# Kernel tuning notes

Hardware: AMD Instinct MI355X
Metric: run time of the kernel (lower is better)

Reference implementation:

```python
import jax, jax.numpy as jnp
import numpy as np

V, D, H, DH, DI, L = 10000, 512, 8, 64, 2048, 12
B, S = 4, 1024
MAX_KLEN = 1024 + 0 + 512  # tgt_len + ext_len + mem_len
EPS = 1e-5
STD = 0.02


def setup_inputs() -> dict:
    key = jax.random.key(0)
    ks = jax.random.split(key, 10)
    data = jax.random.randint(ks[0], (B, S), 0, V)
    word_emb = jax.random.normal(ks[1], (V, D), jnp.float32) * STD
    pos_emb = jax.random.normal(ks[2], (MAX_KLEN, D), jnp.float32) * STD
    Wq = jax.random.normal(ks[3], (L, H * DH, D), jnp.float32) * STD
    Wkv = jax.random.normal(ks[4], (L, 2 * H * DH, D), jnp.float32) * STD
    Wo = jax.random.normal(ks[5], (L, D, H * DH), jnp.float32) * STD
    ln1_g = jnp.ones((L, D), jnp.float32)
    ln1_b = jnp.zeros((L, D), jnp.float32)
    W1 = jax.random.normal(ks[6], (L, DI, D), jnp.float32) * STD
    b1 = jnp.zeros((L, DI), jnp.float32)
    W2 = jax.random.normal(ks[7], (L, D, DI), jnp.float32) * STD
    b2 = jnp.zeros((L, D), jnp.float32)
    ln2_g = jnp.ones((L, D), jnp.float32)
    ln2_b = jnp.zeros((L, D), jnp.float32)
    out_b = jnp.zeros((V,), jnp.float32)  # out_layer weight is tied to word_emb
    return dict(data=data, word_emb=word_emb, pos_emb=pos_emb, Wq=Wq, Wkv=Wkv,
                Wo=Wo, ln1_g=ln1_g, ln1_b=ln1_b, W1=W1, b1=b1, W2=W2, b2=b2,
                ln2_g=ln2_g, ln2_b=ln2_b, out_b=out_b)


def _layernorm(x, g, b):
    m = jnp.mean(x, axis=-1, keepdims=True)
    v = jnp.mean((x - m) ** 2, axis=-1, keepdims=True)
    return (x - m) * jax.lax.rsqrt(v + EPS) * g + b


def reference(data, word_emb, pos_emb, Wq, Wkv, Wo, ln1_g, ln1_b,
              W1, b1, W2, b2, ln2_g, ln2_b, out_b):
    # mems start empty -> mlen = 0, klen = qlen, standard causal mask.
    h = word_emb[data] + pos_emb[:S][None, :, :]      # [B, S, D]
    mask = jnp.triu(jnp.ones((S, S), bool), 1)        # True above diagonal
    scale = 1.0 / np.sqrt(DH)

    def layer(h, p):
        wq, wkv, wo, g1, bl1, w1, bf1, w2, bf2, g2, bl2 = p
        q = (h @ wq.T).reshape(B, S, H, DH)
        k, v = jnp.split(h @ wkv.T, 2, axis=-1)
        k = k.reshape(B, S, H, DH)
        v = v.reshape(B, S, H, DH)
        sc = jnp.einsum('bqhd,bkhd->bhqk', q, k) * scale
        sc = jnp.where(mask[None, None], -jnp.inf, sc)
        p_attn = jax.nn.softmax(sc, axis=-1)           # [B, H, S, S] materialized
        av = jnp.einsum('bhqk,bkhd->bqhd', p_attn, v).reshape(B, S, H * DH)
        h = _layernorm(h + av @ wo.T, g1, bl1)         # post-LN (pre_lnorm=False)
        ff = jax.nn.relu(h @ w1.T + bf1) @ w2.T + bf2
        h = _layernorm(h + ff, g2, bl2)
        return h, None

    h, _ = jax.lax.scan(layer, h,
                        (Wq, Wkv, Wo, ln1_g, ln1_b, W1, b1, W2, b2, ln2_g, ln2_b))
    logits = h @ word_emb.T + out_b                    # tied output projection
    return logits                                      # [B, S, V]
```

## Files before the change

kernel.cpp:

```cpp
#include <hip/hip_runtime.h>

#define VV 10000
#define DD 512
#define HH 8
#define DH 64
#define DI 2048
#define LL 12
#define BB 4
#define SS 1024
#define TT (BB * SS)


typedef __attribute__((ext_vector_type(8))) short bhalf8;
typedef __attribute__((ext_vector_type(16))) float f32x16;

__device__ __forceinline__ void split_bf16(float x, unsigned short& h, unsigned short& l)
{
    unsigned int u = __float_as_uint(x);
    unsigned int r = (u + 0x7FFFu + ((u >> 16) & 1u)) & 0xFFFF0000u;
    h = (unsigned short)(r >> 16);
    float lf = x - __uint_as_float(r);
    unsigned int ul = __float_as_uint(lf);
    l = (unsigned short)((ul + 0x7FFFu + ((ul >> 16) & 1u)) >> 16);
}

__global__ __launch_bounds__(256) void convsplit(
    const float* __restrict__ src, unsigned short* __restrict__ hi,
    unsigned short* __restrict__ lo, int n4)
{
    int stride = gridDim.x * 256;
    for (int i = blockIdx.x * 256 + threadIdx.x; i < n4; i += stride) {
        float4 v = ((const float4*)src)[i];
        ushort4 h, l;
        split_bf16(v.x, h.x, l.x);
        split_bf16(v.y, h.y, l.y);
        split_bf16(v.z, h.z, l.z);
        split_bf16(v.w, h.w, l.w);
        ((ushort4*)hi)[i] = h;
        ((ushort4*)lo)[i] = l;
    }
}

__global__ __launch_bounds__(256) void embed_kernel(
    const int* __restrict__ data, const float* __restrict__ we,
    const float* __restrict__ pe, float* __restrict__ h,
    unsigned short* __restrict__ hhi, unsigned short* __restrict__ hlo)
{
    int tok = blockIdx.x;
    int tid = threadIdx.x;
    int idx = data[tok];
    int s = tok & (SS - 1);
    size_t base = (size_t)tok * DD;
    size_t wb = (size_t)idx * DD;
    size_t pb = (size_t)s * DD;
    float a = we[wb + tid] + pe[pb + tid];
    float b = we[wb + 256 + tid] + pe[pb + 256 + tid];
    h[base + tid] = a;
    h[base + 256 + tid] = b;
    unsigned short hx, lx;
    split_bf16(a, hx, lx); hhi[base + tid] = hx;       hlo[base + tid] = lx;
    split_bf16(b, hx, lx); hhi[base + 256 + tid] = hx; hlo[base + 256 + tid] = lx;
}

template<int BN, int EPI, bool SWZ>
__global__ __launch_bounds__(256) void gemm_mfma(
    const unsigned short* __restrict__ Ahp, const unsigned short* __restrict__ Alp,
    const unsigned short* __restrict__ Whp, const unsigned short* __restrict__ Wlp,
    const float* __restrict__ bias, float* __restrict__ C,
    unsigned short* __restrict__ Chp, unsigned short* __restrict__ Clp,
    unsigned short* __restrict__ Vhp, unsigned short* __restrict__ Vlp,
    int N, int K)
{
    constexpr int FN  = BN / 64;
    constexpr int BT  = BN * 128;
    constexpr int NBG = BN / 8;
    constexpr int NGRP = 32 + 2 * NBG;
    constexpr int PW  = NGRP / 4;
    __shared__ __align__(16) char smem[32768 + 2 * BT];

    int bx = blockIdx.x, by = blockIdx.y;
    if (SWZ) {
        int nwg = gridDim.x * gridDim.y;
        int id = by * gridDim.x + bx;
        int nq = nwg >> 3, rr = nwg & 7;
        int xcd = id & 7, j = id >> 3;
        int nid = (xcd < rr) ? (xcd * (nq + 1) + j)
                             : (rr * (nq + 1) + (xcd - rr) * nq + j);
        bx = nid % gridDim.x;
        by = nid / gridDim.x;
    }

    const int tid   = threadIdx.x;
    const int lane  = tid & 63;
    const int wid   = tid >> 6;
    const int wm    = wid >> 1;
    const int wn    = wid & 1;
    const int laneM = lane & 31;
    const int laneK = lane >> 5;
    const int m0    = by * 128;
    const int n0    = bx * BN;
    const int srow8 = lane >> 3;
    const int sslot = lane & 7;

    f32x16 acc[2][FN];
    #pragma unroll
    for (int i = 0; i < 2; ++i)
        #pragma unroll
        for (int j = 0; j < FN; ++j)
            #pragma unroll
            for (int r = 0; r < 16; ++r) acc[i][j][r] = 0.f;

    for (int k0 = 0; k0 < K; k0 += 64) {
        __syncthreads();
        bhalf8 rbuf[PW];
        #pragma unroll
        for (int t = 0; t < PW; ++t) {
            int g = wid * PW + t;
            const unsigned short* src;
            if (g < 32) {
                const unsigned short* bp = (g < 16) ? Ahp : Alp;
                int row = (g & 15) * 8 + srow8;
                src = bp + (size_t)(m0 + row) * K + (k0 + sslot * 8);
            } else {
                int d = g - 32;
                const unsigned short* bp = (d < NBG) ? Whp : Wlp;
                int row = (d & (NBG - 1)) * 8 + srow8;
                int n = n0 + row;
                n = (n < N) ? n : (N - 1);
                src = bp + (size_t)n * K + (k0 + sslot * 8);
            }
            rbuf[t] = *(const bhalf8*)src;
        }
        #pragma unroll
        for (int t = 0; t < PW; ++t) {
            int g = wid * PW + t;
            int off;
            if (g < 32) {
                int row = (g & 15) * 8 + srow8;
                off = ((g >> 4) << 14) + sslot * 2048 + ((row ^ sslot) << 4);
            } else {
                int d = g - 32;
                int row = (d & (NBG - 1)) * 8 + srow8;
                off = 32768 + ((d < NBG) ? 0 : BT)
                    + sslot * (BN * 16) + ((row ^ sslot) << 4);
            }
            *(bhalf8*)(smem + off) = rbuf[t];
        }
        __syncthreads();

        #pragma unroll
        for (int kb = 0; kb < 4; ++kb) {
            const int slot = kb * 2 + laneK;
            bhalf8 ah[2], al[2], bh[FN], bl[FN];
            #pragma unroll
            for (int i = 0; i < 2; ++i) {
                int row = wm * 64 + i * 32 + laneM;
                int off = slot * 2048 + ((row ^ slot) << 4);
                ah[i] = *(const bhalf8*)(smem + off);
                al[i] = *(const bhalf8*)(smem + 16384 + off);
            }
            #pragma unroll
            for (int j = 0; j < FN; ++j) {
                int row = wn * (BN / 2) + j * 32 + laneM;
                int off = 32768 + slot * (BN * 16) + ((row ^ slot) << 4);
                bh[j] = *(const bhalf8*)(smem + off);
                bl[j] = *(const bhalf8*)(smem + BT + off);
            }
            #pragma unroll
            for (int i = 0; i < 2; ++i)
                #pragma unroll
                for (int j = 0; j < FN; ++j) {
                    acc[i][j] = __builtin_amdgcn_mfma_f32_32x32x16_bf16(ah[i], bh[j], acc[i][j], 0, 0, 0);
                    acc[i][j] = __builtin_amdgcn_mfma_f32_32x32x16_bf16(ah[i], bl[j], acc[i][j], 0, 0, 0);
                    acc[i][j] = __builtin_amdgcn_mfma_f32_32x32x16_bf16(al[i], bh[j], acc[i][j], 0, 0, 0);
                }
        }
    }

    #pragma unroll
    for (int j = 0; j < FN; ++j) {
        int ncol = n0 + wn * (BN / 2) + j * 32 + laneM;
        bool nok = (ncol < N);
        float bv = 0.f;
        if (EPI == 1 || EPI == 2) { if (nok) bv = bias[ncol]; }
        #pragma unroll
        for (int i = 0; i < 2; ++i) {
            #pragma unroll
            for (int r = 0; r < 16; ++r) {
                int mrow = m0 + wm * 64 + i * 32 + (r & 3) + ((r >> 2) << 3) + laneK * 4;
                float v = acc[i][j][r] + bv;
                if (EPI == 2) v = fmaxf(v, 0.f);
                if (nok) {
                    if (EPI == 2 || EPI == 3) {
                        unsigned short hx, lx;
                        split_bf16(v, hx, lx);
                        Chp[(size_t)mrow * N + ncol] = hx;
                        Clp[(size_t)mrow * N + ncol] = lx;
                    } else if (EPI == 4) {
                        unsigned short hx, lx;
                        split_bf16(v, hx, lx);
                        if (ncol < 512) {
                            Chp[(size_t)mrow * 512 + ncol] = hx;
                            Clp[(size_t)mrow * 512 + ncol] = lx;
                        } else {
                            Vhp[(size_t)(ncol - 512) * TT + mrow] = hx;
                            Vlp[(size_t)(ncol - 512) * TT + mrow] = lx;
                        }
                    } else {
                        C[(size_t)mrow * N + ncol] = v;
                    }
                }
            }
        }
    }
}

__global__ __launch_bounds__(128) void flash_mfma(
    const unsigned short* __restrict__ qhp, const unsigned short* __restrict__ qlp,
    const unsigned short* __restrict__ khp, const unsigned short* __restrict__ klp,
    const unsigned short* __restrict__ vthp, const unsigned short* __restrict__ vtlp,
    unsigned short* __restrict__ avh, unsigned short* __restrict__ avl)
{
    __shared__ __align__(16) char lds[50176];

    const int qt  = 15 - (int)blockIdx.x;
    const int hh  = blockIdx.y;
    const int b   = blockIdx.z;
    const int tid = threadIdx.x;
    const int lane  = tid & 63;
    const int wq    = tid >> 6;
    const int laneM = lane & 31;
    const int laneK = lane >> 5;
    const int q0    = qt * 64;

    bhalf8 Qh[4], Ql[4];
    {
        size_t qoff = (size_t)(b * SS + q0 + 32 * wq + laneM) * 512 + hh * 64 + 8 * laneK;
        #pragma unroll
        for (int ks = 0; ks < 4; ++ks) {
            Qh[ks] = *(const bhalf8*)(qhp + qoff + 16 * ks);
            Ql[ks] = *(const bhalf8*)(qlp + qoff + 16 * ks);
        }
    }

    f32x16 O0, O1;
    #pragma unroll
    for (int r = 0; r < 16; ++r) { O0[r] = 0.f; O1[r] = 0.f; }
    float mrun = -1e30f, lrun = 0.f;

    const int srow  = tid >> 1;
    const int shalf = tid & 1;
    float* Pl = (float*)(lds + 32768 + wq * 8704);

    for (int kt = 0; kt <= qt; ++kt) {
        __syncthreads();
        {
            size_t kbase = (size_t)(b * SS + kt * 64 + srow) * 512 + hh * 64 + 32 * shalf;
            size_t vbase = (size_t)(hh * 64 + srow) * TT + b * SS + kt * 64 + 32 * shalf;
            bhalf8 k0[4], k1[4], v0[4], v1[4];
            #pragma unroll
            for (int j = 0; j < 4; ++j) {
                k0[j] = *(const bhalf8*)(khp  + kbase + 8 * j);
                k1[j] = *(const bhalf8*)(klp  + kbase + 8 * j);
                v0[j] = *(const bhalf8*)(vthp + vbase + 8 * j);
                v1[j] = *(const bhalf8*)(vtlp + vbase + 8 * j);
            }
            int ob = srow * 128 + 64 * shalf;
            int sw = (srow & 7) << 4;
            #pragma unroll
            for (int j = 0; j < 4; ++j) {
                int o = (ob + 16 * j) ^ sw;
                *(bhalf8*)(lds + o)         = k0[j];
                *(bhalf8*)(lds + 8192 + o)  = k1[j];
                *(bhalf8*)(lds + 16384 + o) = v0[j];
                *(bhalf8*)(lds + 24576 + o) = v1[j];
            }
        }
        __syncthreads();

        f32x16 s0, s1;
        #pragma unroll
        for (int r = 0; r < 16; ++r) { s0[r] = 0.f; s1[r] = 0.f; }
        #pragma unroll
        for (int ks = 0; ks < 4; ++ks) {
            int db = 32 * ks + 16 * laneK;
            int o0 = (laneM * 128 + db) ^ ((laneM & 7) << 4);
            int r1 = 32 + laneM;
            int o1 = (r1 * 128 + db) ^ ((r1 & 7) << 4);
            bhalf8 kh0 = *(const bhalf8*)(lds + o0);
            bhalf8 kl0 = *(const bhalf8*)(lds + 8192 + o0);
            bhalf8 kh1 = *(const bhalf8*)(lds + o1);
            bhalf8 kl1 = *(const bhalf8*)(lds + 8192 + o1);
            s0 = __builtin_amdgcn_mfma_f32_32x32x16_bf16(kh0, Qh[ks], s0, 0, 0, 0);
            s0 = __builtin_amdgcn_mfma_f32_32x32x16_bf16(kh0, Ql[ks], s0, 0, 0, 0);
            s0 = __builtin_amdgcn_mfma_f32_32x32x16_bf16(kl0, Qh[ks], s0, 0, 0, 0);
            s1 = __builtin_amdgcn_mfma_f32_32x32x16_bf16(kh1, Qh[ks], s1, 0, 0, 0);
            s1 = __builtin_amdgcn_mfma_f32_32x32x16_bf16(kh1, Ql[ks], s1, 0, 0, 0);
            s1 = __builtin_amdgcn_mfma_f32_32x32x16_bf16(kl1, Qh[ks], s1, 0, 0, 0);
        }

        #pragma unroll
        for (int r = 0; r < 16; ++r) { s0[r] *= 0.125f; s1[r] *= 0.125f; }

        if (kt == qt) {
            int qrel = 32 * wq + laneM;
            #pragma unroll
            for (int r = 0; r < 16; ++r) {
                int krel = (r & 3) + ((r >> 2) << 3) + 4 * laneK;
                if (krel > qrel)      s0[r] = -1e30f;
                if (krel + 32 > qrel) s1[r] = -1e30f;
            }
        }

        float mx = s0[0];
        #pragma unroll
        for (int r = 1; r < 16; ++r) mx = fmaxf(mx, s0[r]);
        #pragma unroll
        for (int r = 0; r < 16; ++r) mx = fmaxf(mx, s1[r]);
        mx = fmaxf(mx, __shfl_xor(mx, 32));
        float mn = fmaxf(mrun, mx);
        float alpha = __expf(mrun - mn);
        mrun = mn;
        float rs = 0.f;
        #pragma unroll
        for (int r = 0; r < 16; ++r) {
            float p0 = __expf(s0[r] - mn);
            float p1 = __expf(s1[r] - mn);
            s0[r] = p0; s1[r] = p1;
            rs += p0 + p1;
        }
        rs += __shfl_xor(rs, 32);
        lrun = lrun * alpha + rs;
        #pragma unroll
        for (int r = 0; r < 16; ++r) { O0[r] *= alpha; O1[r] *= alpha; }

        #pragma unroll
        for (int r = 0; r < 16; ++r) {
            int krel = (r & 3) + ((r >> 2) << 3) + 4 * laneK;
            Pl[laneM * 68 + krel]      = s0[r];
            Pl[laneM * 68 + 32 + krel] = s1[r];
        }
        __asm__ volatile("s_waitcnt lgkmcnt(0)" ::: "memory");
        __builtin_amdgcn_sched_barrier(0);

        #pragma unroll
        for (int ks = 0; ks < 4; ++ks) {
            const float* pr = &Pl[laneM * 68 + 16 * ks + 8 * laneK];
            float4 pa = *(const float4*)pr;
            float4 pb = *(const float4*)(pr + 4);
            float pv[8] = {pa.x, pa.y, pa.z, pa.w, pb.x, pb.y, pb.z, pb.w};
            bhalf8 ph, plo;
            #pragma unroll
            for (int i = 0; i < 8; ++i) {
                unsigned u = __float_as_uint(pv[i]);
                ph[i] = (short)(u >> 16);
                float lf = pv[i] - __uint_as_float(u & 0xFFFF0000u);
                plo[i] = (short)(__float_as_uint(lf) >> 16);
            }
            int db = 32 * ks + 16 * laneK;
            {
                int col = laneM;
                int o = (col * 128 + db) ^ ((col & 7) << 4);
                bhalf8 vh = *(const bhalf8*)(lds + 16384 + o);
                bhalf8 vl = *(const bhalf8*)(lds + 24576 + o);
                O0 = __builtin_amdgcn_mfma_f32_32x32x16_bf16(vh, ph,  O0, 0, 0, 0);
                O0 = __builtin_amdgcn_mfma_f32_32x32x16_bf16(vl, ph,  O0, 0, 0, 0);
                O0 = __builtin_amdgcn_mfma_f32_32x32x16_bf16(vh, plo, O0, 0, 0, 0);
            }
            {
                int col = 32 + laneM;
                int o = (col * 128 + db) ^ ((col & 7) << 4);
                bhalf8 vh = *(const bhalf8*)(lds + 16384 + o);
                bhalf8 vl = *(const bhalf8*)(lds + 24576 + o);
                O1 = __builtin_amdgcn_mfma_f32_32x32x16_bf16(vh, ph,  O1, 0, 0, 0);
                O1 = __builtin_amdgcn_mfma_f32_32x32x16_bf16(vl, ph,  O1, 0, 0, 0);
                O1 = __builtin_amdgcn_mfma_f32_32x32x16_bf16(vh, plo, O1, 0, 0, 0);
            }
        }
    }

    float inv = 1.0f / lrun;
    #pragma unroll
    for (int r = 0; r < 16; ++r) {
        int d = (r & 3) + ((r >> 2) << 3) + 4 * laneK;
        Pl[laneM * 68 + d]      = O0[r] * inv;
        Pl[laneM * 68 + 32 + d] = O1[r] * inv;
    }
    __asm__ volatile("s_waitcnt lgkmcnt(0)" ::: "memory");
    __builtin_amdgcn_sched_barrier(0);
    #pragma unroll
    for (int it = 0; it < 16; ++it) {
        int qr = it * 2 + (lane >> 5);
        int d  = (lane & 31) * 2;
        float2 v = *(const float2*)&Pl[qr * 68 + d];
        unsigned short h0, l0, h1, l1;
        split_bf16(v.x, h0, l0);
        split_bf16(v.y, h1, l1);
        size_t base = (size_t)(b * SS + q0 + 32 * wq + qr) * 512 + hh * 64 + d;
        ushort2 hv; hv.x = h0; hv.y = h1;
        ushort2 lv; lv.x = l0; lv.y = l1;
        *(ushort2*)(avh + base) = hv;
        *(ushort2*)(avl + base) = lv;
    }
}

__global__ __launch_bounds__(256) void add_ln_kernel(
    float* __restrict__ h, const float* __restrict__ x,
    const float* __restrict__ g, const float* __restrict__ bta,
    unsigned short* __restrict__ hhi, unsigned short* __restrict__ hlo)
{
    int tok = blockIdx.x, tid = threadIdx.x;
    size_t base = (size_t)tok * DD;
    float v0 = h[base + tid] + x[base + tid];
    float v1 = h[base + 256 + tid] + x[base + 256 + tid];

    __shared__ float rs[256], rq[256];
    rs[tid] = v0 + v1;
    rq[tid] = v0 * v0 + v1 * v1;
    __syncthreads();
    for (int off = 128; off > 0; off >>= 1) {
        if (tid < off) { rs[tid] += rs[tid + off]; rq[tid] += rq[tid + off]; }
        __syncthreads();
    }
    float mean = rs[0] * (1.f / 512.f);
    float var  = rq[0] * (1.f / 512.f) - mean * mean;
    float inv  = rsqrtf(var + 1e-5f);
    float o0 = (v0 - mean) * inv * g[tid]       + bta[tid];
    float o1 = (v1 - mean) * inv * g[256 + tid] + bta[256 + tid];
    h[base + tid]       = o0;
    h[base + 256 + tid] = o1;
    unsigned short a, b;
    split_bf16(o0, a, b); hhi[base + tid]       = a; hlo[base + tid]       = b;
    split_bf16(o1, a, b); hhi[base + 256 + tid] = a; hlo[base + 256 + tid] = b;
}

extern "C" void kernel_launch(void* const* d_in, const int* in_sizes, int n_in,
                              void* d_out, int out_size, void* d_ws, size_t ws_size,
                              hipStream_t stream)
{
    const int*   data = (const int*)d_in[0];
    const float* we   = (const float*)d_in[1];
    const float* pe   = (const float*)d_in[2];
    const float* Wq   = (const float*)d_in[3];
    const float* Wkv  = (const float*)d_in[4];
    const float* Wo   = (const float*)d_in[5];
    const float* g1   = (const float*)d_in[6];
    const float* bl1  = (const float*)d_in[7];
    const float* W1   = (const float*)d_in[8];
    const float* b1   = (const float*)d_in[9];
    const float* W2   = (const float*)d_in[10];
    const float* b2   = (const float*)d_in[11];
    const float* g2   = (const float*)d_in[12];
    const float* bl2  = (const float*)d_in[13];
    const float* outb = (const float*)d_in[14];
    float* out = (float*)d_out;

    typedef unsigned short us;
    float* h    = (float*)d_ws;
    us* qhp  = (us*)(h + (size_t)TT * 512);
    us* qlp  = qhp  + (size_t)TT * 512;
    us* khp  = qlp  + (size_t)TT * 512;
    us* klp  = khp  + (size_t)TT * 512;
    us* vthp = klp  + (size_t)TT * 512;
    us* vtlp = vthp + (size_t)TT * 512;
    us* avh  = vtlp + (size_t)TT * 512;
    us* avl  = avh  + (size_t)TT * 512;
    float* tmp = (float*)(avl + (size_t)TT * 512);
    us* hhi  = (us*)(tmp + (size_t)TT * 512);
    us* hlo  = hhi + (size_t)TT * 512;
    us* ffh = qhp;
    us* ffl = qhp + (size_t)TT * 2048;
    us* wqh  = hlo + (size_t)TT * 512;
    us* wql  = wqh  + (size_t)LL * 512 * 512;
    us* wkvh = wql  + (size_t)LL * 512 * 512;
    us* wkvl = wkvh + (size_t)LL * 1024 * 512;
    us* woh  = wkvl + (size_t)LL * 1024 * 512;
    us* wol  = woh  + (size_t)LL * 512 * 512;
    us* w1h  = wol  + (size_t)LL * 512 * 512;
    us* w1l  = w1h  + (size_t)LL * 2048 * 512;
    us* w2h  = w1l  + (size_t)LL * 2048 * 512;
    us* w2l  = w2h  + (size_t)LL * 512 * 2048;
    us* weh  = w2l  + (size_t)LL * 512 * 2048;
    us* wel  = weh  + (size_t)VV * 512;

    auto cv = [&](const float* s, us* hh, us* ll, size_t n) {
        int n4 = (int)(n >> 2);
        int blocks = (n4 + 255) / 256;
        if (blocks > 2048) blocks = 2048;
        convsplit<<<blocks, 256, 0, stream>>>(s, hh, ll, n4);
    };
    cv(Wq,  wqh,  wql,  (size_t)LL * 512 * 512);
    cv(Wkv, wkvh, wkvl, (size_t)LL * 1024 * 512);
    cv(Wo,  woh,  wol,  (size_t)LL * 512 * 512);
    cv(W1,  w1h,  w1l,  (size_t)LL * 2048 * 512);
    cv(W2,  w2h,  w2l,  (size_t)LL * 512 * 2048);
    cv(we,  weh,  wel,  (size_t)VV * 512);

    embed_kernel<<<TT, 256, 0, stream>>>(data, we, pe, h, hhi, hlo);

    for (int l = 0; l < LL; ++l) {
        const us* lwqh  = wqh  + (size_t)l * 512 * 512;
        const us* lwql  = wql  + (size_t)l * 512 * 512;
        const us* lwkvh = wkvh + (size_t)l * 1024 * 512;
        const us* lwkvl = wkvl + (size_t)l * 1024 * 512;
        const us* lwoh  = woh  + (size_t)l * 512 * 512;
        const us* lwol  = wol  + (size_t)l * 512 * 512;
        const us* lw1h  = w1h  + (size_t)l * 2048 * 512;
        const us* lw1l  = w1l  + (size_t)l * 2048 * 512;
        const us* lw2h  = w2h  + (size_t)l * 512 * 2048;
        const us* lw2l  = w2l  + (size_t)l * 512 * 2048;

        gemm_mfma<64, 3, false><<<dim3(8, 32), 256, 0, stream>>>(
            hhi, hlo, lwqh, lwql, nullptr, nullptr, qhp, qlp, nullptr, nullptr, 512, 512);
        gemm_mfma<128, 4, false><<<dim3(8, 32), 256, 0, stream>>>(
            hhi, hlo, lwkvh, lwkvl, nullptr, nullptr, khp, klp, vthp, vtlp, 1024, 512);
        flash_mfma<<<dim3(16, HH, BB), 128, 0, stream>>>(
            qhp, qlp, khp, klp, vthp, vtlp, avh, avl);
        gemm_mfma<64, 0, false><<<dim3(8, 32), 256, 0, stream>>>(
            avh, avl, lwoh, lwol, nullptr, tmp, nullptr, nullptr, nullptr, nullptr, 512, 512);
        add_ln_kernel<<<TT, 256, 0, stream>>>(h, tmp, g1 + l * 512, bl1 + l * 512, hhi, hlo);
        gemm_mfma<128, 2, false><<<dim3(16, 32), 256, 0, stream>>>(
            hhi, hlo, lw1h, lw1l, b1 + l * 2048, nullptr, ffh, ffl, nullptr, nullptr, 2048, 512);
        gemm_mfma<64, 1, false><<<dim3(8, 32), 256, 0, stream>>>(
            ffh, ffl, lw2h, lw2l, b2 + l * 512, tmp, nullptr, nullptr, nullptr, nullptr, 512, 2048);
        add_ln_kernel<<<TT, 256, 0, stream>>>(h, tmp, g2 + l * 512, bl2 + l * 512, hhi, hlo);
    }

    gemm_mfma<128, 1, true><<<dim3((VV + 127) / 128, 32), 256, 0, stream>>>(
        hhi, hlo, weh, wel, outb, out, nullptr, nullptr, nullptr, nullptr, VV, 512);
}
```

Baseline: 3.500 ms.

## Prefetch GEMM tiles into registers, hardcode XCD swizzle, raise MFMA priority

The GEMM main loop now issues next-iteration global loads into registers right after the LDS store, so they overlap with the MFMA compute. Load offsets and LDS addresses are precomputed once, using 32-bit offsets from the Ahp base. The XCD-aware block swizzle is replaced by a hardcoded mapping that assumes a 79-wide grid with 10-column groups. Attention MFMA sections are wrapped in s_setprio to favor matrix-issuing waves. The hardcoded swizzle only fits one grid shape and may mis-map blocks for any other SWZ launch, and the int offsets could overflow on large buffers.

```diff
diff --git a/kernel.cpp b/kernel.cpp
--- a/kernel.cpp
+++ b/kernel.cpp
@@ -80,14 +80,10 @@
 
     int bx = blockIdx.x, by = blockIdx.y;
     if (SWZ) {
-        int nwg = gridDim.x * gridDim.y;
-        int id = by * gridDim.x + bx;
-        int nq = nwg >> 3, rr = nwg & 7;
-        int xcd = id & 7, j = id >> 3;
-        int nid = (xcd < rr) ? (xcd * (nq + 1) + j)
-                             : (rr * (nq + 1) + (xcd - rr) * nq + j);
-        bx = nid % gridDim.x;
-        by = nid / gridDim.x;
+        int id = by * 79 + bx;
+        int t  = (id & 7) * 316 + (id >> 3);
+        if (t < 2240) { int c = t / 320, r = t - c * 320; by = r / 10; bx = c * 10 + r % 10; }
+        else          { int r = t - 2240;                 by = r / 9;  bx = 70 + r % 9; }
     }
 
     const int tid   = threadIdx.x;
@@ -102,6 +98,29 @@
     const int srow8 = lane >> 3;
     const int sslot = lane & 7;
 
+    const int dAl = (int)(Alp - Ahp);
+    const int dW  = (int)(Whp - Ahp);
+    const int dWl = (int)(Wlp - Ahp);
+    int offs[PW];
+    int ldso[PW];
+    #pragma unroll
+    for (int t = 0; t < PW; ++t) {
+        int g = wid * PW + t;
+        if (g < 32) {
+            int row = (g & 15) * 8 + srow8;
+            offs[t] = (g < 16 ? 0 : dAl) + (m0 + row) * K + sslot * 8;
+            ldso[t] = ((g >> 4) << 14) + sslot * 2048 + ((row ^ sslot) << 4);
+        } else {
+            int d = g - 32;
+            int row = (d & (NBG - 1)) * 8 + srow8;
+            int n = n0 + row;
+            n = (n < N) ? n : (N - 1);
+            offs[t] = (d < NBG ? dW : dWl) + n * K + sslot * 8;
+            ldso[t] = 32768 + ((d < NBG) ? 0 : BT)
+                    + sslot * (BN * 16) + ((row ^ sslot) << 4);
+        }
+    }
+
     f32x16 acc[2][FN];
     #pragma unroll
     for (int i = 0; i < 2; ++i)
@@ -109,44 +128,24 @@
         for (int j = 0; j < FN; ++j)
             #pragma unroll
             for (int r = 0; r < 16; ++r) acc[i][j][r] = 0.f;
+
+    bhalf8 rbuf[PW];
+    #pragma unroll
+    for (int t = 0; t < PW; ++t)
+        rbuf[t] = *(const bhalf8*)(Ahp + offs[t]);
 
     for (int k0 = 0; k0 < K; k0 += 64) {
         __syncthreads();
-        bhalf8 rbuf[PW];
-        #pragma unroll
-        for (int t = 0; t < PW; ++t) {
-            int g = wid * PW + t;
-            const unsigned short* src;
-            if (g < 32) {
-                const unsigned short* bp = (g < 16) ? Ahp : Alp;
-                int row = (g & 15) * 8 + srow8;
-                src = bp + (size_t)(m0 + row) * K + (k0 + sslot * 8);
-            } else {
-                int d = g - 32;
-                const unsigned short* bp = (d < NBG) ? Whp : Wlp;
-                int row = (d & (NBG - 1)) * 8 + srow8;
-                int n = n0 + row;
-                n = (n < N) ? n : (N - 1);
-                src = bp + (size_t)n * K + (k0 + sslot * 8);
-            }
-            rbuf[t] = *(const bhalf8*)src;
-        }
-        #pragma unroll
-        for (int t = 0; t < PW; ++t) {
-            int g = wid * PW + t;
-            int off;
-            if (g < 32) {
-                int row = (g & 15) * 8 + srow8;
-                off = ((g >> 4) << 14) + sslot * 2048 + ((row ^ sslot) << 4);
-            } else {
-                int d = g - 32;
-                int row = (d & (NBG - 1)) * 8 + srow8;
-                off = 32768 + ((d < NBG) ? 0 : BT)
-                    + sslot * (BN * 16) + ((row ^ sslot) << 4);
-            }
-            *(bhalf8*)(smem + off) = rbuf[t];
-        }
+        #pragma unroll
+        for (int t = 0; t < PW; ++t)
+            *(bhalf8*)(smem + ldso[t]) = rbuf[t];
         __syncthreads();
+
+        if (k0 + 64 < K) {
+            #pragma unroll
+            for (int t = 0; t < PW; ++t)
+                rbuf[t] = *(const bhalf8*)(Ahp + offs[t] + k0 + 64);
+        }
 
         #pragma unroll
         for (int kb = 0; kb < 4; ++kb) {
@@ -281,6 +280,7 @@
         f32x16 s0, s1;
         #pragma unroll
         for (int r = 0; r < 16; ++r) { s0[r] = 0.f; s1[r] = 0.f; }
+        __builtin_amdgcn_s_setprio(1);
         #pragma unroll
         for (int ks = 0; ks < 4; ++ks) {
             int db = 32 * ks + 16 * laneK;
@@ -298,6 +298,7 @@
             s1 = __builtin_amdgcn_mfma_f32_32x32x16_bf16(kh1, Ql[ks], s1, 0, 0, 0);
             s1 = __builtin_amdgcn_mfma_f32_32x32x16_bf16(kl1, Qh[ks], s1, 0, 0, 0);
         }
+        __builtin_amdgcn_s_setprio(0);
 
         #pragma unroll
         for (int r = 0; r < 16; ++r) { s0[r] *= 0.125f; s1[r] *= 0.125f; }
@@ -358,6 +359,7 @@
                 plo[i] = (short)(__float_as_uint(lf) >> 16);
             }
             int db = 32 * ks + 16 * laneK;
+            __builtin_amdgcn_s_setprio(1);
             {
                 int col = laneM;
                 int o = (col * 128 + db) ^ ((col & 7) << 4);
@@ -376,6 +378,7 @@
                 O1 = __builtin_amdgcn_mfma_f32_32x32x16_bf16(vl, ph,  O1, 0, 0, 0);
                 O1 = __builtin_amdgcn_mfma_f32_32x32x16_bf16(vh, plo, O1, 0, 0, 0);
             }
+            __builtin_amdgcn_s_setprio(0);
         }
     }
 
```

Measured after the change: 3.218 ms. 8.1% less time.
